# Performance work log

Hardware: AMD Instinct MI355X
Metric: run time of the kernel (lower is better)

Reference implementation:

```python
import math
import jax, jax.numpy as jnp
import numpy as np

HIDDEN = 2048
N_HEAD = 32
N_KV = 8
HEAD_DIM = HIDDEN // N_HEAD  # 64
B, S = 2, 2048


def setup_inputs() -> dict:
    key = jax.random.key(0)
    ks = jax.random.split(key, 9)
    sc_h = 1.0 / math.sqrt(HIDDEN)
    return {
        "X": jax.random.normal(ks[0], (B, S, HIDDEN), jnp.float32),
        "Wq": jax.random.normal(ks[1], (HIDDEN, HIDDEN), jnp.float32) * sc_h,
        "bq": jax.random.normal(ks[2], (HIDDEN,), jnp.float32) * 0.01,
        "Wk": jax.random.normal(ks[3], (N_KV * HEAD_DIM, HIDDEN), jnp.float32) * sc_h,
        "bk": jax.random.normal(ks[4], (N_KV * HEAD_DIM,), jnp.float32) * 0.01,
        "Wv": jax.random.normal(ks[5], (N_KV * HEAD_DIM, HIDDEN), jnp.float32) * sc_h,
        "bv": jax.random.normal(ks[6], (N_KV * HEAD_DIM,), jnp.float32) * 0.01,
        "Wo": jax.random.normal(ks[7], (HIDDEN, HIDDEN), jnp.float32) * sc_h,
        "bo": jax.random.normal(ks[8], (HIDDEN,), jnp.float32) * 0.01,
    }


def reference(X, Wq, bq, Wk, bk, Wv, bv, Wo, bo):
    b, s, _ = X.shape
    g = N_HEAD // N_KV  # query heads per kv head (repeat_interleave group)
    scale = 1.0 / math.sqrt(HEAD_DIM)

    q = X @ Wq.T + bq                       # [B,S,H*D]
    k = X @ Wk.T + bk                       # [B,S,KV*D]
    v = X @ Wv.T + bv                       # [B,S,KV*D]

    # q grouped as (B, KV, g, S, D): head h = kv*g + j matches repeat_interleave on dim=1
    q = q.reshape(b, s, N_KV, g, HEAD_DIM).transpose(0, 2, 3, 1, 4)  # [B,KV,g,S,D]
    k = k.reshape(b, s, N_KV, HEAD_DIM).transpose(0, 2, 1, 3)         # [B,KV,S,D]
    v = v.reshape(b, s, N_KV, HEAD_DIM).transpose(0, 2, 1, 3)         # [B,KV,S,D]

    # scores without materializing repeated K/V: broadcast kv head over g query heads
    scores = jnp.einsum("bkgqd,bkld->bkgql", q, k) * scale            # [B,KV,g,S,S]
    weights = jax.nn.softmax(scores, axis=-1)
    out = jnp.einsum("bkgql,bkld->bkgqd", weights, v)                 # [B,KV,g,S,D]

    # replicate torch's contiguous .view(B, seq, -1) applied to the [B,H,S,D]
    # tensor WITHOUT transposing back: plain row-major reshape of (B,H,S,D).
    out = out.reshape(b, s, N_HEAD * HEAD_DIM)
    return out @ Wo.T + bo
```

## Files before the change

kernel.cpp:

```cpp
#include <hip/hip_runtime.h>

#define HIDDEN 2048
#define NHEADS 32
#define NKV    8
#define HDIM   64
#define BATCH  2
#define SEQ    2048
#define MROWS  (BATCH*SEQ)
#define NQKV   3072

#define SCALEQ 0.18033688011112042f

typedef _Float16 half8_t __attribute__((ext_vector_type(8)));
typedef _Float16 half4_t __attribute__((ext_vector_type(4)));
typedef __fp16   fp16x2_t __attribute__((ext_vector_type(2)));
typedef float    f32x4_t __attribute__((ext_vector_type(4)));

#define AS1 __attribute__((address_space(1)))
#define AS3 __attribute__((address_space(3)))

__device__ __forceinline__ void async_copy16(void* lds, const void* g) {
    __builtin_amdgcn_global_load_lds((AS1 void*)g, (AS3 void*)lds, 16, 0, 0);
}

template <typename OutT, bool QKV>
__global__ __launch_bounds__(256) void gemm_nt(
    const _Float16* __restrict__ A, const _Float16* __restrict__ Bm,
    const float* __restrict__ bias, OutT* __restrict__ C,
    _Float16* __restrict__ kfb, _Float16* __restrict__ vfb,
    int M, int N, int K, int ldc) {
    __shared__ _Float16 As[2][128 * 32];
    __shared__ _Float16 Bs[2][128 * 32];

    const int tid  = threadIdx.x;
    const int wave = tid >> 6;
    const int lane = tid & 63;
    const int quad = lane >> 4;
    const int l16  = lane & 15;
    const int m0 = blockIdx.y * 128;
    const int n0 = blockIdx.x * 128;
    const int mw = (wave & 1) * 64;
    const int nw = (wave >> 1) * 64;

    f32x4_t acc[4][4] = {};

    const int srow = tid >> 2;
    const int scol = (tid & 3) * 8;
    const _Float16* Ag = A  + (size_t)(m0 + srow) * K + scol;
    const _Float16* Bg = Bm + (size_t)(n0 + srow) * K + scol;
    const int woff = wave * 512;

    async_copy16(&As[0][woff],        Ag);
    async_copy16(&As[0][woff + 2048], Ag + (size_t)64 * K);
    async_copy16(&Bs[0][woff],        Bg);
    async_copy16(&Bs[0][woff + 2048], Bg + (size_t)64 * K);

    const int iters = K >> 5;
    for (int it = 0; it < iters; ++it) {
        __syncthreads();
        const int cur = it & 1;
        if (it + 1 < iters) {
            const int nxt = cur ^ 1;
            const int k1 = (it + 1) << 5;
            async_copy16(&As[nxt][woff],        Ag + k1);
            async_copy16(&As[nxt][woff + 2048], Ag + (size_t)64 * K + k1);
            async_copy16(&Bs[nxt][woff],        Bg + k1);
            async_copy16(&Bs[nxt][woff + 2048], Bg + (size_t)64 * K + k1);
        }

        half8_t a[4], b[4];
#pragma unroll
        for (int i = 0; i < 4; ++i)
            a[i] = *(const half8_t*)(&As[cur][(mw + i * 16 + l16) * 32 + quad * 8]);
#pragma unroll
        for (int i = 0; i < 4; ++i)
            b[i] = *(const half8_t*)(&Bs[cur][(nw + i * 16 + l16) * 32 + quad * 8]);
#pragma unroll
        for (int mi = 0; mi < 4; ++mi)
#pragma unroll
            for (int ni = 0; ni < 4; ++ni)
                acc[mi][ni] = __builtin_amdgcn_mfma_f32_16x16x32_f16(
                    a[mi], b[ni], acc[mi][ni], 0, 0, 0);
    }

    if (QKV && n0 >= 2560) {
#pragma unroll
        for (int mi = 0; mi < 4; ++mi) {
#pragma unroll
            for (int ni = 0; ni < 4; ++ni) {
                const int c  = n0 + nw + ni * 16 + l16;
                const int kd = c - 2560;
                const int kv = kd >> 6, d = kd & 63;
                const float bv = bias[c];
                const int r0 = m0 + mw + mi * 16 + quad * 4;
                const int bb = r0 >> 11;
                const int sblk = (r0 & 2047) >> 6;
                const int nt = (r0 >> 4) & 3;
                const int dt = (d >> 4) & 3;
                half4_t h;
#pragma unroll
                for (int i = 0; i < 4; ++i) h[i] = (_Float16)(acc[mi][ni][i] + bv);
                *(half4_t*)(vfb + ((size_t)(bb * 8 + kv) * 32 + sblk) * 4096 +
                            ((nt * 4 + dt) * 64 + quad * 16 + (d & 15)) * 4) = h;
            }
        }
    } else if (QKV && n0 >= 2048) {
#pragma unroll
        for (int mi = 0; mi < 4; ++mi) {
#pragma unroll
            for (int ni = 0; ni < 4; ++ni) {
                const int c  = n0 + nw + ni * 16 + l16;
                const int kd = c - 2048;
                const int kv = kd >> 6, d = kd & 63;
                const float bv = bias[c];
                const int r0 = m0 + mw + mi * 16 + quad * 4;
                const int bb = r0 >> 11;
                const int sblk = (r0 & 2047) >> 6;
                const int nt = (r0 >> 4) & 3;
                _Float16* dst = kfb + ((size_t)(bb * 8 + kv) * 32 + sblk) * 4096 +
                    ((nt * 2 + (d >> 5)) * 64 + ((d >> 3) & 3) * 16 + quad * 4) * 8 +
                    (d & 7);
#pragma unroll
                for (int i = 0; i < 4; ++i)
                    dst[i * 8] = (_Float16)(acc[mi][ni][i] + bv);
            }
        }
    } else {
#pragma unroll
        for (int mi = 0; mi < 4; ++mi) {
#pragma unroll
            for (int ni = 0; ni < 4; ++ni) {
                const int c = n0 + nw + ni * 16 + l16;
                const float bv = bias[c];
#pragma unroll
                for (int i = 0; i < 4; ++i) {
                    const int r = m0 + mw + mi * 16 + quad * 4 + i;
                    C[(size_t)r * ldc + c] = (OutT)(acc[mi][ni][i] + bv);
                }
            }
        }
    }
}

__global__ __launch_bounds__(256, 2) void attn_kernel(
    const _Float16* __restrict__ Qb, const _Float16* __restrict__ Kf,
    const _Float16* __restrict__ Vf, _Float16* __restrict__ ctx) {
    __shared__ _Float16 Ks[2][4096];
    __shared__ _Float16 Vs[2][4096];

    const int tid  = threadIdx.x;
    const int wave = tid >> 6;
    const int lane = tid & 63;
    const int quad = lane >> 4;
    const int l16  = lane & 15;
    const int qt  = blockIdx.x;
    const int bkv = blockIdx.y;
    const int b   = bkv >> 3;
    const int kv  = bkv & 7;
    const int h   = kv * 4 + wave;

    half8_t qa[4][2];
#pragma unroll
    for (int g = 0; g < 4; ++g) {
        const _Float16* qp = Qb + ((size_t)(b * SEQ + qt * 64 + g * 16 + l16)) * HIDDEN
                              + h * 64 + quad * 8;
        qa[g][0] = *(const half8_t*)qp;
        qa[g][1] = *(const half8_t*)(qp + 32);
    }

    f32x4_t ot[4][4] = {};
    f32x4_t lacc[4] = {};
    const half4_t ones = {(_Float16)1.f, (_Float16)1.f, (_Float16)1.f, (_Float16)1.f};

    const size_t kvbase = (size_t)(b * 8 + kv) * 32 * 4096;
    const int sh = (wave * 2) * 512 + lane * 8;

#pragma unroll
    for (int j = 0; j < 2; ++j) {
        async_copy16(&Ks[0][(wave * 2 + j) * 512], Kf + kvbase + sh + j * 512);
        async_copy16(&Vs[0][(wave * 2 + j) * 512], Vf + kvbase + sh + j * 512);
    }

    for (int kt = 0; kt < SEQ / 64; ++kt) {
        __syncthreads();
        const int cur = kt & 1;
        if (kt + 1 < SEQ / 64) {
            const int nxt = cur ^ 1;
            const size_t off = kvbase + (size_t)(kt + 1) * 4096 + sh;
#pragma unroll
            for (int j = 0; j < 2; ++j) {
                async_copy16(&Ks[nxt][(wave * 2 + j) * 512], Kf + off + j * 512);
                async_copy16(&Vs[nxt][(wave * 2 + j) * 512], Vf + off + j * 512);
            }
        }

        half8_t kf[4][2];
#pragma unroll
        for (int nt = 0; nt < 4; ++nt) {
#pragma unroll
            for (int c = 0; c < 2; ++c)
                kf[nt][c] = *(const half8_t*)(&Ks[cur][((nt * 2 + c) * 64 + lane) * 8]);
        }

        half4_t p[4][4];
#pragma unroll
        for (int g = 0; g < 4; ++g) {
#pragma unroll
            for (int nt = 0; nt < 4; ++nt) {
                f32x4_t s = {};
                s = __builtin_amdgcn_mfma_f32_16x16x32_f16(kf[nt][0], qa[g][0], s, 0, 0, 0);
                s = __builtin_amdgcn_mfma_f32_16x16x32_f16(kf[nt][1], qa[g][1], s, 0, 0, 0);
                const fp16x2_t lo = __builtin_amdgcn_cvt_pkrtz(
                    __builtin_amdgcn_exp2f(s[0]), __builtin_amdgcn_exp2f(s[1]));
                const fp16x2_t hi = __builtin_amdgcn_cvt_pkrtz(
                    __builtin_amdgcn_exp2f(s[2]), __builtin_amdgcn_exp2f(s[3]));
                half4_t pv;
                pv[0] = (_Float16)lo[0]; pv[1] = (_Float16)lo[1];
                pv[2] = (_Float16)hi[0]; pv[3] = (_Float16)hi[1];
                p[g][nt] = pv;
                lacc[g] = __builtin_amdgcn_mfma_f32_16x16x16f16(ones, pv, lacc[g], 0, 0, 0);
            }
        }

#pragma unroll
        for (int nt = 0; nt < 4; ++nt) {
#pragma unroll
            for (int dt = 0; dt < 4; ++dt) {
                const half4_t vf = *(const half4_t*)(&Vs[cur][((nt * 4 + dt) * 64 + lane) * 4]);
#pragma unroll
                for (int g = 0; g < 4; ++g)
                    ot[g][dt] = __builtin_amdgcn_mfma_f32_16x16x16f16(
                        vf, p[g][nt], ot[g][dt], 0, 0, 0);
            }
        }
    }

    __syncthreads();
    _Float16* T = &Ks[0][0] + wave * 1152;
#pragma unroll
    for (int g = 0; g < 4; ++g) {
        const float inv = 1.f / lacc[g][0];
#pragma unroll
        for (int dt = 0; dt < 4; ++dt) {
            half4_t hh;
#pragma unroll
            for (int r = 0; r < 4; ++r) hh[r] = (_Float16)(ot[g][dt][r] * inv);
            *(half4_t*)(T + l16 * 72 + dt * 16 + quad * 4) = hh;
        }
        __builtin_amdgcn_s_waitcnt(0);
        _Float16* cp = ctx + (((size_t)b * 32 + h) * SEQ + qt * 64 + g * 16 + l16) * 64;
#pragma unroll
        for (int pass = 0; pass < 2; ++pass) {
            const half8_t row = *(const half8_t*)(T + l16 * 72 + pass * 32 + quad * 8);
            *(half8_t*)(cp + pass * 32 + quad * 8) = row;
        }
        __builtin_amdgcn_s_waitcnt(0);
    }
}

__device__ __forceinline__ void cast4(const float* __restrict__ s,
                                      _Float16* __restrict__ d, int i, float sc) {
    const f32x4_t v = ((const f32x4_t*)s)[i];
    half4_t h;
#pragma unroll
    for (int j = 0; j < 4; ++j) h[j] = (_Float16)(v[j] * sc);
    ((half4_t*)d)[i] = h;
}

__global__ __launch_bounds__(256) void prep(
    const float* __restrict__ X,  const float* __restrict__ Wq,
    const float* __restrict__ Wk, const float* __restrict__ Wv,
    const float* __restrict__ Wo, const float* __restrict__ bq,
    const float* __restrict__ bk, const float* __restrict__ bv,
    _Float16* __restrict__ Xh, _Float16* __restrict__ Wqkv,
    _Float16* __restrict__ Woh, float* __restrict__ bqkv) {
    const int bid = blockIdx.x, tid = threadIdx.x;
    if (bid < 8192)       cast4(X,  Xh,   bid * 256 + tid, 1.f);
    else if (bid < 12288) cast4(Wq, Wqkv, (bid - 8192) * 256 + tid, SCALEQ);
    else if (bid < 13312) cast4(Wk, Wqkv + (size_t)HIDDEN * HIDDEN, (bid - 12288) * 256 + tid, 1.f);
    else if (bid < 14336) cast4(Wv, Wqkv + (size_t)(HIDDEN + 512) * HIDDEN, (bid - 13312) * 256 + tid, 1.f);
    else if (bid < 18432) cast4(Wo, Woh,  (bid - 14336) * 256 + tid, 1.f);
    else {
        const int i = (bid - 18432) * 256 + tid;
        if (i < 2048)      bqkv[i] = bq[i] * SCALEQ;
        else if (i < 2560) bqkv[i] = bk[i - 2048];
        else if (i < 3072) bqkv[i] = bv[i - 2560];
    }
}

extern "C" void kernel_launch(void* const* d_in, const int* in_sizes, int n_in,
                              void* d_out, int out_size, void* d_ws, size_t ws_size,
                              hipStream_t stream) {
    const float* X  = (const float*)d_in[0];
    const float* Wq = (const float*)d_in[1];
    const float* bq = (const float*)d_in[2];
    const float* Wk = (const float*)d_in[3];
    const float* bk = (const float*)d_in[4];
    const float* Wv = (const float*)d_in[5];
    const float* bv = (const float*)d_in[6];
    const float* Wo = (const float*)d_in[7];
    const float* bo = (const float*)d_in[8];
    float* out = (float*)d_out;

    char* p = (char*)d_ws;
    _Float16* Xh   = (_Float16*)p; p += (size_t)MROWS * HIDDEN * 2;
    _Float16* Wqkv = (_Float16*)p; p += (size_t)NQKV * HIDDEN * 2;
    _Float16* Woh  = (_Float16*)p; p += (size_t)HIDDEN * HIDDEN * 2;
    float*    bqkv = (float*)p;    p += (size_t)NQKV * 4;
    _Float16* Qb   = (_Float16*)p; p += (size_t)MROWS * HIDDEN * 2;
    _Float16* Kfb  = (_Float16*)p; p += (size_t)16 * 32 * 4096 * 2;
    _Float16* Vfb  = (_Float16*)p; p += (size_t)16 * 32 * 4096 * 2;
    _Float16* ctx  = Xh;

    prep<<<18444, 256, 0, stream>>>(X, Wq, Wk, Wv, Wo, bq, bk, bv,
                                    Xh, Wqkv, Woh, bqkv);

    gemm_nt<_Float16, true><<<dim3(NQKV / 128, MROWS / 128), 256, 0, stream>>>(
        Xh, Wqkv, bqkv, Qb, Kfb, Vfb, MROWS, NQKV, HIDDEN, HIDDEN);

    attn_kernel<<<dim3(SEQ / 64, BATCH * NKV), 256, 0, stream>>>(Qb, Kfb, Vfb, ctx);

    gemm_nt<float, false><<<dim3(HIDDEN / 128, MROWS / 128), 256, 0, stream>>>(
        ctx, Woh, bo, out, nullptr, nullptr, MROWS, HIDDEN, HIDDEN, HIDDEN);
}
```

Baseline: 335.2 us.

## Replace 128x128 GEMM with 256x256 tiled, swizzled, ping-pong scheduled GEMM

Rewrites both projection GEMMs to use 256x256 output tiles with 8 waves, a 64-wide K step, XOR-swizzled LDS layout to avoid bank conflicts, and a workgroup-index remap across XCDs. The main loop interleaves staged async global-to-LDS loads with MFMA quarters, separated by barriers and s_setprio, to overlap memory and compute. Larger tiles cut global traffic per FLOP but reduce grid size (e.g. 12x16 and 8x16 blocks) and raise register and LDS pressure, which may leave CUs underused.

```diff
diff --git a/kernel.cpp b/kernel.cpp
--- a/kernel.cpp
+++ b/kernel.cpp
@@ -23,80 +23,154 @@
     __builtin_amdgcn_global_load_lds((AS1 void*)g, (AS3 void*)lds, 16, 0, 0);
 }
 
+#define PRIO1 __builtin_amdgcn_s_setprio(1)
+#define PRIO0 __builtin_amdgcn_s_setprio(0)
+#define BAR   __builtin_amdgcn_s_barrier()
+
+
+#define LDA(dst, bi, mh) do {                                                  \
+    _Pragma("unroll") for (int mi = 0; mi < 4; ++mi) {                         \
+        dst[mi][0] = *(const half8_t*)(&As[bi][abase + (mh)*4096 + mi*1024 + g0]); \
+        dst[mi][1] = *(const half8_t*)(&As[bi][abase + (mh)*4096 + mi*1024 + g1]); \
+    } } while (0)
+
+#define LDB(dst, bi) do {                                                      \
+    _Pragma("unroll") for (int ni = 0; ni < 4; ++ni) {                         \
+        dst[ni][0] = *(const half8_t*)(&Bs[bi][bbase + ni*1024 + g0]);         \
+        dst[ni][1] = *(const half8_t*)(&Bs[bi][bbase + ni*1024 + g1]);         \
+    } } while (0)
+
+#define MFMA_Q(av, bv, mh, nh) do {                                            \
+    _Pragma("unroll") for (int mi = 0; mi < 4; ++mi)                           \
+    _Pragma("unroll") for (int ni = 0; ni < 2; ++ni) {                         \
+        f32x4_t& cc = acc[(mh)*4 + mi][(nh)*2 + ni];                           \
+        cc = __builtin_amdgcn_mfma_f32_16x16x32_f16(av[mi][0], bv[(nh)*2+ni][0], cc, 0, 0, 0); \
+        cc = __builtin_amdgcn_mfma_f32_16x16x32_f16(av[mi][1], bv[(nh)*2+ni][1], cc, 0, 0, 0); \
+    } } while (0)
+
+#define STG_AH(bi, hf, kb) do {                                                \
+    async_copy16(&As[bi][(hf)*8192 + ldst],        Ag + (size_t)((hf)*128)      * K + (kb)); \
+    async_copy16(&As[bi][(hf)*8192 + 4096 + ldst], Ag + (size_t)((hf)*128 + 64) * K + (kb)); \
+  } while (0)
+#define STG_BH(bi, hf, kb) do {                                                \
+    async_copy16(&Bs[bi][(hf)*8192 + ldst],        Bg + (size_t)((hf)*128)      * K + (kb)); \
+    async_copy16(&Bs[bi][(hf)*8192 + 4096 + ldst], Bg + (size_t)((hf)*128 + 64) * K + (kb)); \
+  } while (0)
+
 template <typename OutT, bool QKV>
-__global__ __launch_bounds__(256) void gemm_nt(
+__global__ __launch_bounds__(512, 2) void gemm256(
     const _Float16* __restrict__ A, const _Float16* __restrict__ Bm,
     const float* __restrict__ bias, OutT* __restrict__ C,
     _Float16* __restrict__ kfb, _Float16* __restrict__ vfb,
-    int M, int N, int K, int ldc) {
-    __shared__ _Float16 As[2][128 * 32];
-    __shared__ _Float16 Bs[2][128 * 32];
+    int K, int ldc) {
+    __shared__ _Float16 As[2][16384];
+    __shared__ _Float16 Bs[2][16384];
 
     const int tid  = threadIdx.x;
     const int wave = tid >> 6;
     const int lane = tid & 63;
     const int quad = lane >> 4;
     const int l16  = lane & 15;
-    const int m0 = blockIdx.y * 128;
-    const int n0 = blockIdx.x * 128;
-    const int mw = (wave & 1) * 64;
-    const int nw = (wave >> 1) * 64;
-
-    f32x4_t acc[4][4] = {};
-
-    const int srow = tid >> 2;
-    const int scol = (tid & 3) * 8;
-    const _Float16* Ag = A  + (size_t)(m0 + srow) * K + scol;
-    const _Float16* Bg = Bm + (size_t)(n0 + srow) * K + scol;
-    const int woff = wave * 512;
-
-    async_copy16(&As[0][woff],        Ag);
-    async_copy16(&As[0][woff + 2048], Ag + (size_t)64 * K);
-    async_copy16(&Bs[0][woff],        Bg);
-    async_copy16(&Bs[0][woff + 2048], Bg + (size_t)64 * K);
-
-    const int iters = K >> 5;
-    for (int it = 0; it < iters; ++it) {
-        __syncthreads();
-        const int cur = it & 1;
-        if (it + 1 < iters) {
-            const int nxt = cur ^ 1;
-            const int k1 = (it + 1) << 5;
-            async_copy16(&As[nxt][woff],        Ag + k1);
-            async_copy16(&As[nxt][woff + 2048], Ag + (size_t)64 * K + k1);
-            async_copy16(&Bs[nxt][woff],        Bg + k1);
-            async_copy16(&Bs[nxt][woff + 2048], Bg + (size_t)64 * K + k1);
-        }
-
-        half8_t a[4], b[4];
-#pragma unroll
-        for (int i = 0; i < 4; ++i)
-            a[i] = *(const half8_t*)(&As[cur][(mw + i * 16 + l16) * 32 + quad * 8]);
-#pragma unroll
-        for (int i = 0; i < 4; ++i)
-            b[i] = *(const half8_t*)(&Bs[cur][(nw + i * 16 + l16) * 32 + quad * 8]);
-#pragma unroll
-        for (int mi = 0; mi < 4; ++mi)
-#pragma unroll
-            for (int ni = 0; ni < 4; ++ni)
-                acc[mi][ni] = __builtin_amdgcn_mfma_f32_16x16x32_f16(
-                    a[mi], b[ni], acc[mi][ni], 0, 0, 0);
+    const int wr   = wave >> 2;
+    const int wc   = wave & 3;
+
+    const int nwg = (int)(gridDim.x * gridDim.y);
+    const int lin = (int)(blockIdx.y * gridDim.x + blockIdx.x);
+    const int q8  = nwg >> 3;
+    const int idx = (lin & 7) * q8 + (lin >> 3);
+    const int tx  = idx % (int)gridDim.x;
+    const int ty  = idx / (int)gridDim.x;
+    const int m0  = ty * 256;
+    const int n0  = tx * 256;
+
+    const int srow = tid >> 3;
+    const int sg   = ((tid & 7) ^ (srow & 7)) << 3;
+    const _Float16* Ag = A  + (size_t)(m0 + srow) * K + sg;
+    const _Float16* Bg = Bm + (size_t)(n0 + srow) * K + sg;
+    const int ldst = wave * 512;
+
+    const int sk = l16 & 7;
+    const int g0 = ((0 + quad) ^ sk) << 3;
+    const int g1 = ((4 + quad) ^ sk) << 3;
+    const int abase = wr * 8192 + l16 * 64;
+    const int bbase = wc * 4096 + l16 * 64;
+
+    f32x4_t acc[8][4] = {};
+
+    const int NT    = K >> 6;
+    const int iters = NT >> 1;
+
+    STG_AH(0, 0, 0);  STG_AH(0, 1, 0);  STG_BH(0, 0, 0);  STG_BH(0, 1, 0);
+    STG_AH(1, 0, 64); STG_AH(1, 1, 64); STG_BH(1, 0, 64); STG_BH(1, 1, 64);
+    asm volatile("s_waitcnt vmcnt(8)" ::: "memory");
+    BAR;
+
+    for (int i = 0; i < iters; ++i) {
+        const int  kb1 = (2 * i + 1) << 6;
+        const int  kb2 = (2 * i + 2) << 6;
+        const int  kb3 = (2 * i + 3) << 6;
+        const bool nx  = (i + 1 < iters);
+        half8_t a[4][2], a2[4][2], b[4][2];
+
+        LDA(a, 0, 0);
+        LDB(b, 0);
+        if (i > 0) STG_AH(1, 1, kb1);
+        BAR;
+        PRIO1; MFMA_Q(a, b, 0, 0); PRIO0;
+        BAR;
+        LDA(a2, 0, 1);
+        if (nx) STG_BH(0, 0, kb2);
+        BAR;
+        PRIO1; MFMA_Q(a, b, 0, 1); PRIO0;
+        BAR;
+        if (nx) STG_BH(0, 1, kb2);
+        BAR;
+        PRIO1; MFMA_Q(a2, b, 1, 1); PRIO0;
+        BAR;
+        if (nx) STG_AH(0, 0, kb2);
+        BAR;
+        PRIO1; MFMA_Q(a2, b, 1, 0); PRIO0;
+        if (nx) { asm volatile("s_waitcnt vmcnt(6)" ::: "memory"); }
+        else    { asm volatile("s_waitcnt vmcnt(0)" ::: "memory"); }
+        BAR;
+
+        LDA(a, 1, 0);
+        LDB(b, 1);
+        if (nx) STG_AH(0, 1, kb2);
+        BAR;
+        PRIO1; MFMA_Q(a, b, 0, 0); PRIO0;
+        BAR;
+        LDA(a2, 1, 1);
+        if (nx) STG_BH(1, 0, kb3);
+        BAR;
+        PRIO1; MFMA_Q(a, b, 0, 1); PRIO0;
+        BAR;
+        if (nx) STG_BH(1, 1, kb3);
+        BAR;
+        PRIO1; MFMA_Q(a2, b, 1, 1); PRIO0;
+        BAR;
+        if (nx) STG_AH(1, 0, kb3);
+        BAR;
+        PRIO1; MFMA_Q(a2, b, 1, 0); PRIO0;
+        if (nx) { asm volatile("s_waitcnt vmcnt(6)" ::: "memory"); }
+        else    { asm volatile("s_waitcnt vmcnt(0)" ::: "memory"); }
+        BAR;
     }
 
     if (QKV && n0 >= 2560) {
 #pragma unroll
-        for (int mi = 0; mi < 4; ++mi) {
-#pragma unroll
-            for (int ni = 0; ni < 4; ++ni) {
-                const int c  = n0 + nw + ni * 16 + l16;
-                const int kd = c - 2560;
-                const int kv = kd >> 6, d = kd & 63;
-                const float bv = bias[c];
-                const int r0 = m0 + mw + mi * 16 + quad * 4;
-                const int bb = r0 >> 11;
+        for (int ni = 0; ni < 4; ++ni) {
+            const int c  = n0 + wc * 64 + ni * 16 + l16;
+            const int kd = c - 2560;
+            const int kv = kd >> 6, d = kd & 63;
+            const int dt = (d >> 4) & 3;
+            const float bv = bias[c];
+#pragma unroll
+            for (int mi = 0; mi < 8; ++mi) {
+                const int r0   = m0 + wr * 128 + mi * 16 + quad * 4;
+                const int bb   = r0 >> 11;
                 const int sblk = (r0 & 2047) >> 6;
-                const int nt = (r0 >> 4) & 3;
-                const int dt = (d >> 4) & 3;
+                const int nt   = (r0 >> 4) & 3;
                 half4_t h;
 #pragma unroll
                 for (int i = 0; i < 4; ++i) h[i] = (_Float16)(acc[mi][ni][i] + bv);
@@ -106,17 +180,17 @@
         }
     } else if (QKV && n0 >= 2048) {
 #pragma unroll
-        for (int mi = 0; mi < 4; ++mi) {
-#pragma unroll
-            for (int ni = 0; ni < 4; ++ni) {
-                const int c  = n0 + nw + ni * 16 + l16;
-                const int kd = c - 2048;
-                const int kv = kd >> 6, d = kd & 63;
-                const float bv = bias[c];
-                const int r0 = m0 + mw + mi * 16 + quad * 4;
-                const int bb = r0 >> 11;
+        for (int ni = 0; ni < 4; ++ni) {
+            const int c  = n0 + wc * 64 + ni * 16 + l16;
+            const int kd = c - 2048;
+            const int kv = kd >> 6, d = kd & 63;
+            const float bv = bias[c];
+#pragma unroll
+            for (int mi = 0; mi < 8; ++mi) {
+                const int r0   = m0 + wr * 128 + mi * 16 + quad * 4;
+                const int bb   = r0 >> 11;
                 const int sblk = (r0 & 2047) >> 6;
-                const int nt = (r0 >> 4) & 3;
+                const int nt   = (r0 >> 4) & 3;
                 _Float16* dst = kfb + ((size_t)(bb * 8 + kv) * 32 + sblk) * 4096 +
                     ((nt * 2 + (d >> 5)) * 64 + ((d >> 3) & 3) * 16 + quad * 4) * 8 +
                     (d & 7);
@@ -127,16 +201,15 @@
         }
     } else {
 #pragma unroll
-        for (int mi = 0; mi < 4; ++mi) {
-#pragma unroll
-            for (int ni = 0; ni < 4; ++ni) {
-                const int c = n0 + nw + ni * 16 + l16;
-                const float bv = bias[c];
-#pragma unroll
-                for (int i = 0; i < 4; ++i) {
-                    const int r = m0 + mw + mi * 16 + quad * 4 + i;
-                    C[(size_t)r * ldc + c] = (OutT)(acc[mi][ni][i] + bv);
-                }
+        for (int ni = 0; ni < 4; ++ni) {
+            const int c  = n0 + wc * 64 + ni * 16 + l16;
+            const float bv = bias[c];
+#pragma unroll
+            for (int mi = 0; mi < 8; ++mi) {
+                const int r0 = m0 + wr * 128 + mi * 16 + quad * 4;
+#pragma unroll
+                for (int i = 0; i < 4; ++i)
+                    C[(size_t)(r0 + i) * ldc + c] = (OutT)(acc[mi][ni][i] + bv);
             }
         }
     }
@@ -315,11 +388,11 @@
     prep<<<18444, 256, 0, stream>>>(X, Wq, Wk, Wv, Wo, bq, bk, bv,
                                     Xh, Wqkv, Woh, bqkv);
 
-    gemm_nt<_Float16, true><<<dim3(NQKV / 128, MROWS / 128), 256, 0, stream>>>(
-        Xh, Wqkv, bqkv, Qb, Kfb, Vfb, MROWS, NQKV, HIDDEN, HIDDEN);
+    gemm256<_Float16, true><<<dim3(NQKV / 256, MROWS / 256), 512, 0, stream>>>(
+        Xh, Wqkv, bqkv, Qb, Kfb, Vfb, HIDDEN, HIDDEN);
 
     attn_kernel<<<dim3(SEQ / 64, BATCH * NKV), 256, 0, stream>>>(Qb, Kfb, Vfb, ctx);
 
-    gemm_nt<float, false><<<dim3(HIDDEN / 128, MROWS / 128), 256, 0, stream>>>(
-        ctx, Woh, bo, out, nullptr, nullptr, MROWS, HIDDEN, HIDDEN, HIDDEN);
-}
+    gemm256<float, false><<<dim3(HIDDEN / 256, MROWS / 256), 512, 0, stream>>>(
+        ctx, Woh, bo, out, nullptr, nullptr, HIDDEN, HIDDEN);
+}
```

Measured after the change: 348.0 us. 1.04x slower.
